# Performance work log

Measured on AMD Instinct MI355X. Metric: run time of the kernel, lower is better.

## Reference

```python
import jax, jax.numpy as jnp
import numpy as np

B, H, C = 131072, 16, 32        # batch, n_holidays, n_changepoints
HID, HP, SKU = 512, 512 // 16, 64  # hidden_dim, hidden per holiday, sku embed dim
TEMP = 0.7
TIME_MAX = 365.0
LN_EPS = 1e-3  # keras LayerNormalization default epsilon


def mish(x):
    return x * jnp.tanh(jax.nn.softplus(x))


def setup_inputs() -> dict:
    key = jax.random.key(0)
    ks = jax.random.split(key, 12)
    inputs = jax.random.uniform(ks[0], (B, H), dtype=jnp.float32) * TIME_MAX
    sku_embedding = jax.random.normal(ks[1], (B, SKU), dtype=jnp.float32)
    # per-holiday params, stacked over holiday axis
    deltas = jnp.full((H, C), TIME_MAX / C, dtype=jnp.float32)  # changepoint_deltas init
    ln_gamma = jnp.ones((H, C), dtype=jnp.float32)
    ln_beta = jnp.zeros((H, C), dtype=jnp.float32)
    attn_w = jax.random.normal(ks[2], (H,), dtype=jnp.float32) * 0.5  # Dense(1) on [...,1]
    Wh = jax.random.normal(ks[3], (H, C, HP), dtype=jnp.float32) * (1.0 / np.sqrt(C))
    Wah = jax.random.normal(ks[4], (HID, HID), dtype=jnp.float32) * (1.0 / np.sqrt(HID))
    Waa = jax.random.normal(ks[5], (HID, HID), dtype=jnp.float32) * (1.0 / np.sqrt(HID))
    Wb = jax.random.normal(ks[6], (SKU, HID), dtype=jnp.float32) * (1.0 / np.sqrt(SKU))
    Wa = jax.random.normal(ks[7], (SKU, HID), dtype=jnp.float32) * (1.0 / np.sqrt(SKU))
    Wo = jax.random.normal(ks[8], (HID, 1), dtype=jnp.float32)
    Wo = Wo / jnp.linalg.norm(Wo, axis=0, keepdims=True)  # UnitNorm(axis=0) constraint
    return {"inputs": inputs, "sku_embedding": sku_embedding, "deltas": deltas,
            "ln_gamma": ln_gamma, "ln_beta": ln_beta, "attn_w": attn_w, "Wh": Wh,
            "Wah": Wah, "Waa": Waa, "Wb": Wb, "Wa": Wa, "Wo": Wo}


def reference(inputs, sku_embedding, deltas, ln_gamma, ln_beta, attn_w, Wh, Wah, Waa, Wb, Wa, Wo):
    # ChangepointReLU (vectorised over holidays): softplus -> cumsum -> rescale to [0, 365]
    pd = jax.nn.softplus(deltas)                     # [H, C]
    cps = jnp.cumsum(pd, axis=-1)
    cps = cps / cps[:, -1:] * TIME_MAX               # time_min = 0
    feats = jax.nn.relu(inputs[:, :, None] - cps[None, :, :])  # [B, H, C]
    # per-holiday LayerNorm over changepoint axis
    mu = jnp.mean(feats, axis=-1, keepdims=True)
    var = jnp.mean((feats - mu) ** 2, axis=-1, keepdims=True)
    normed = (feats - mu) * jax.lax.rsqrt(var + LN_EPS) * ln_gamma[None] + ln_beta[None]
    # per-holiday attention: Dense(1,no bias) on [...,1] == scalar multiply per holiday
    logits = normed * attn_w[None, :, None]
    attn = jax.nn.softmax(logits / TEMP, axis=-1)    # n_changepoints > 1
    attended = normed * attn                          # [B, H, C]
    # per-holiday hidden Dense(HP, mish, no bias), then concat over holidays
    hid = mish(jnp.einsum('bhc,hcd->bhd', attended, Wh))  # [B, H, HP]
    aggregated = hid.reshape(hid.shape[0], H * HP)        # [B, HID]
    agg_hidden = mish(aggregated @ Wah)                   # [B, HID]
    agg_attn = jax.nn.softmax((agg_hidden @ Waa) / TEMP, axis=-1)
    final = agg_hidden * agg_attn                         # dropout inactive (inference)
    beta = jax.nn.sigmoid(sku_embedding @ Wb)
    alpha = sku_embedding @ Wa
    final = final * beta + alpha
    return final @ Wo                                     # [B, 1]
```

## Files before the change

kernel.cpp:

```cpp
#include <hip/hip_runtime.h>
#include <hip/hip_fp16.h>
#include <stdint.h>

#define B_TOT 131072
#define CHUNK 65536
#define NH 16
#define NC 32
#define HIDD 512

typedef unsigned short u16;
typedef unsigned int u32;
typedef __attribute__((ext_vector_type(8))) short short8;
typedef __attribute__((ext_vector_type(4))) float f32x4;
typedef __attribute__((ext_vector_type(4))) int i32x4;

#define GLLDS(g, l) __builtin_amdgcn_global_load_lds((const __attribute__((address_space(1))) unsigned int*)(g), (__attribute__((address_space(3))) unsigned int*)(l), 16, 0, 0)

__device__ __forceinline__ u16 f2bf(float x){
  unsigned u = __float_as_uint(x);
  u += 0x7fffu + ((u >> 16) & 1u);
  return (u16)(u >> 16);
}
__device__ __forceinline__ float bf2f(u16 b){ return __uint_as_float(((unsigned)b) << 16); }
__device__ __forceinline__ u16 f2h(float x){ __half h = __float2half(x); return *(u16*)&h; }
__device__ __forceinline__ float h2f(u16 b){ __half h; *(u16*)&h = b; return __half2float(h); }
__device__ __forceinline__ float mishf(float x){
  float e = __expf(fminf(x, 30.f));
  float u = 1.f + e;
  float u2 = u * u;
  return x * (u2 - 1.f) * __builtin_amdgcn_rcpf(u2 + 1.f);
}

__global__ void prep_small(const float* __restrict__ deltas, const float* __restrict__ Wa,
                           const float* __restrict__ Wo, float* __restrict__ cps, float* __restrict__ wWo)
{
  const int t = threadIdx.x;
  if (t < NH){
    float cum[NC];
    float run = 0.f;
#pragma unroll
    for (int c = 0; c < NC; c++){
      float d = deltas[t*NC + c];
      float sp = (d > 20.f) ? d : log1pf(__expf(d));
      run += sp; cum[c] = run;
    }
    float s = 365.0f / run;
#pragma unroll
    for (int c = 0; c < NC; c++) cps[t*NC + c] = cum[c] * s;
  } else if (t >= 64 && t < 128){
    const int k = t - 64;
    float s = 0.f;
    for (int n = 0; n < HIDD; n++) s += Wa[k*HIDD + n] * Wo[n];
    wWo[k] = s;
  }
}

__global__ void prep_convert(const float* __restrict__ Wah, const float* __restrict__ Waa,
                             const float* __restrict__ Wb, const float* __restrict__ Wh,
                             u16* __restrict__ WahT, u16* __restrict__ WaaT,
                             u16* __restrict__ WbT, u16* __restrict__ WhT)
{
  int i = blockIdx.x * 256 + threadIdx.x;
  if (i < 262144){ int n = i >> 9, k = i & 511; WahT[i] = f2bf(Wah[k*512 + n]); return; }
  i -= 262144;
  if (i < 262144){ int n = i >> 9, k = i & 511; WaaT[i] = f2bf(Waa[k*512 + n]); return; }
  i -= 262144;
  if (i < 32768){ int n = i >> 6, k = i & 63; WbT[i] = f2bf(Wb[k*512 + n]); return; }
  i -= 32768;
  if (i < 16384){ int h = i >> 10, r = i & 1023, d = r >> 5, c = r & 31;
                  WhT[i] = f2bf(Wh[h*1024 + c*32 + d]); return; }
}

__global__ __launch_bounds__(256) void stage1_kernel(
    const float* __restrict__ inputs, const float* __restrict__ sku,
    const float* __restrict__ ln_g, const float* __restrict__ ln_b,
    const float* __restrict__ attnw, const float* __restrict__ cps,
    const float* __restrict__ wWo, const u16* __restrict__ WhT,
    u16* __restrict__ agg, u16* __restrict__ skub, float* __restrict__ skd)
{
  __shared__ __align__(16) float in_l[256];
  __shared__ __align__(16) float cps_l[512];
  __shared__ __align__(16) float gam_l[512];
  __shared__ __align__(16) float bet_l[512];
  __shared__ float aw_l[16];
  __shared__ __align__(16) u16 at_l[16*16*32];
  __shared__ __align__(16) u16 ot_l[16*512];

  const int t = threadIdx.x;
  const int ln = t & 63;
  const long bb = (long)blockIdx.x * 64;

  cps_l[t] = cps[t];       cps_l[t+256] = cps[t+256];
  gam_l[t] = ln_g[t];      gam_l[t+256] = ln_g[t+256];
  bet_l[t] = ln_b[t];      bet_l[t+256] = ln_b[t+256];
  if (t < 16) aw_l[t] = attnw[t];
  in_l[t] = inputs[bb*16 + t];

#pragma unroll
  for (int it = 0; it < 4; it++){
    const long bs = bb + it*16;
    const f32x4 sv = *(const f32x4*)&sku[bs*64 + t*4];
    unsigned lo = (unsigned)f2bf(sv.x) | ((unsigned)f2bf(sv.y) << 16);
    unsigned hi = (unsigned)f2bf(sv.z) | ((unsigned)f2bf(sv.w) << 16);
    unsigned long long v = (unsigned long long)lo | ((unsigned long long)hi << 32);
    *(unsigned long long*)&skub[bs*64 + t*4] = v;
    const f32x4 wv4 = *(const f32x4*)&wWo[(ln & 15)*4];
    float pd = sv.x*wv4.x + sv.y*wv4.y + sv.z*wv4.z + sv.w*wv4.w;
#pragma unroll
    for (int s = 1; s < 16; s <<= 1) pd += __shfl_xor(pd, s);
    if ((ln & 15) == 0) skd[bs + (t >> 4)] = pd;
  }

  const int h = t >> 4, bi = t & 15;
  const int wv = t >> 6;
  const int lrow = ln & 15, lq = ln >> 4;

  short8 wf0[4], wf1[4];
#pragma unroll
  for (int q = 0; q < 4; q++){
    const int hh = wv*4 + q;
    wf0[q] = *(const short8*)&WhT[hh*1024 + lrow*32 + lq*8];
    wf1[q] = *(const short8*)&WhT[hh*1024 + (16 + lrow)*32 + lq*8];
  }
  __syncthreads();

#pragma unroll 1
  for (int it = 0; it < 4; it++){
    const float x = in_l[bi*16 + h];
    const float awv = aw_l[h] * (1.0f/0.7f);
    float nrm[NC];
    float s1 = 0.f;
#pragma unroll
    for (int c = 0; c < NC; c++){ float f = fmaxf(x - cps_l[h*NC + c], 0.f); nrm[c] = f; s1 += f; }
    const float mu = s1 * (1.f/NC);
    float s2 = 0.f;
#pragma unroll
    for (int c = 0; c < NC; c++){ float d = nrm[c] - mu; s2 += d*d; }
    const float rs = rsqrtf(s2 * (1.f/NC) + 1e-3f);
    float lmax = -1e30f;
#pragma unroll
    for (int c = 0; c < NC; c++){
      float nv = (nrm[c] - mu) * rs * gam_l[h*NC + c] + bet_l[h*NC + c];
      nrm[c] = nv;
      lmax = fmaxf(lmax, nv * awv);
    }
    float ps = 0.f;
#pragma unroll
    for (int c = 0; c < NC; c++) ps += __expf(nrm[c]*awv - lmax);
    const float invs = __builtin_amdgcn_rcpf(ps);
#pragma unroll
    for (int c = 0; c < NC; c += 2){
      const float p0 = __expf(nrm[c]*awv - lmax) * invs;
      const float p1 = __expf(nrm[c+1]*awv - lmax) * invs;
      unsigned pk = (unsigned)f2bf(nrm[c]*p0) | ((unsigned)f2bf(nrm[c+1]*p1) << 16);
      *(unsigned*)&at_l[h*512 + bi*32 + c] = pk;
    }
    __syncthreads();

    if (it < 3) in_l[t] = inputs[(bb + (it+1)*16)*16 + t];

#pragma unroll
    for (int q = 0; q < 4; q++){
      const int hh = wv*4 + q;
      short8 af = *(const short8*)&at_l[hh*512 + lrow*32 + lq*8];
      f32x4 acc0 = {0.f,0.f,0.f,0.f}, acc1 = {0.f,0.f,0.f,0.f};
      acc0 = __builtin_amdgcn_mfma_f32_16x16x32_bf16(af, wf0[q], acc0, 0, 0, 0);
      acc1 = __builtin_amdgcn_mfma_f32_16x16x32_bf16(af, wf1[q], acc1, 0, 0, 0);
#pragma unroll
      for (int r = 0; r < 4; r++){
        const int br = lq*4 + r;
        ot_l[br*512 + hh*32 + lrow]      = f2bf(mishf(acc0[r]));
        ot_l[br*512 + hh*32 + 16 + lrow] = f2bf(mishf(acc1[r]));
      }
    }
    __syncthreads();

    {
      const int row = t >> 4, c16 = t & 15;
      const i32x4* src = (const i32x4*)&ot_l[row*512 + c16*32];
      i32x4* dst = (i32x4*)&agg[(bb + it*16 + row)*512 + c16*32];
#pragma unroll
      for (int j = 0; j < 4; j++) dst[j] = src[j];
    }
    __syncthreads();
  }
}

__global__ __launch_bounds__(256, 3) void gemm1(
    const u16* __restrict__ A, const u16* __restrict__ Bt, u16* __restrict__ aggh)
{
  __shared__ __align__(16) u16 smem[24576];
  const int t = threadIdx.x, wv = t >> 6, ln = t & 63;
  const int g = blockIdx.x;
  const int m_idx = (g & 7) + ((g >> 5) << 3);
  const int n_idx = (g >> 3) & 3;
  const long m0 = (long)m_idx * 128;
  const int n0 = n_idx * 128;
  const int lrow = ln & 15, lq = ln >> 4;
  const int wm = wv >> 1, wn = wv & 1;

  auto stage = [&](int buf, int kt){
#pragma unroll
    for (int p = 0; p < 2; p++){
      const int chunk = p*256 + wv*64 + ln;
      const int mm = chunk >> 2, kc = chunk & 3;
      const int kcl = kc ^ ((mm >> 1) & 3);
      GLLDS(&A[(m0 + mm)*512 + kt + kcl*8],  &smem[buf*4096 + (p*256 + wv*64)*8]);
      GLLDS(&Bt[(n0 + mm)*512 + kt + kcl*8], &smem[12288 + buf*4096 + (p*256 + wv*64)*8]);
    }
  };

  f32x4 acc[4][4] = {};
  stage(0, 0); stage(1, 32);
#pragma unroll 1
  for (int ks = 0; ks < 16; ks++){
    const int cur = ks % 3;
    if (ks < 15) asm volatile("s_waitcnt vmcnt(4)" ::: "memory");
    else         asm volatile("s_waitcnt vmcnt(0)" ::: "memory");
    __builtin_amdgcn_s_barrier();
    if (ks + 2 < 16) stage((ks + 2) % 3, (ks + 2)*32);
    short8 a[4], b[4];
#pragma unroll
    for (int i = 0; i < 4; i++){
      const int ra = wm*64 + i*16 + lrow;
      const int rb = wn*64 + i*16 + lrow;
      const int lqa = lq ^ ((ra >> 1) & 3);
      const int lqb = lq ^ ((rb >> 1) & 3);
      a[i] = *(const short8*)&smem[cur*4096 + ra*32 + lqa*8];
      b[i] = *(const short8*)&smem[12288 + cur*4096 + rb*32 + lqb*8];
    }
#pragma unroll
    for (int i = 0; i < 4; i++)
#pragma unroll
      for (int j = 0; j < 4; j++)
        acc[i][j] = __builtin_amdgcn_mfma_f32_16x16x32_bf16(a[i], b[j], acc[i][j], 0, 0, 0);
  }

  const int TP = 136;
  __syncthreads();
#pragma unroll 1
  for (int h = 0; h < 2; h++){
    if (wm == h){
#pragma unroll
      for (int i = 0; i < 4; i++)
#pragma unroll
        for (int j = 0; j < 4; j++)
#pragma unroll
          for (int r = 0; r < 4; r++)
            smem[(i*16 + lq*4 + r)*TP + wn*64 + j*16 + lrow] = f2bf(mishf(acc[i][j][r]));
    }
    __syncthreads();
#pragma unroll
    for (int it = 0; it < 4; it++){
      const int idx = it*256 + t;
      const int row = idx >> 4, ch = idx & 15;
      const i32x4 v = *(const i32x4*)&smem[row*TP + ch*8];
      *(i32x4*)&aggh[(m0 + h*64 + row)*512 + n0 + ch*8] = v;
    }
    __syncthreads();
  }
}

__global__ __launch_bounds__(256, 3) void mega2f(
    const u16* __restrict__ A, const u16* __restrict__ Bt,
    const u16* __restrict__ skub, const u16* __restrict__ WbT,
    const float* __restrict__ Wo, float* __restrict__ part)
{
  __shared__ __align__(16) u16 smem[24576];
  const int t = threadIdx.x, wv = t >> 6, ln = t & 63;
  const int g = blockIdx.x;
  const int m_idx = (g & 7) + ((g >> 5) << 3);
  const int n_idx = (g >> 3) & 3;
  const long m0 = (long)m_idx * 128;
  const int n0 = n_idx * 128;
  const int lrow = ln & 15, lq = ln >> 4;
  const int wm = wv >> 1, wn = wv & 1;
  const float inv_t = 1.0f / 0.7f;

  u32 bwp[4][4][2];
  {
    auto stage3 = [&](int buf, int kt){
#pragma unroll
      for (int p = 0; p < 2; p++){
        const int chunk = p*256 + wv*64 + ln;
        const int mm = chunk >> 2, kc = chunk & 3;
        const int kcl = kc ^ ((mm >> 1) & 3);
        GLLDS(&skub[(m0 + mm)*64 + kt + kcl*8], &smem[buf*4096 + (p*256 + wv*64)*8]);
        GLLDS(&WbT[(n0 + mm)*64 + kt + kcl*8],  &smem[8192 + buf*4096 + (p*256 + wv*64)*8]);
      }
    };
    f32x4 acc3[4][4] = {};
    stage3(0, 0); stage3(1, 32);
    asm volatile("s_waitcnt vmcnt(0)" ::: "memory");
    __builtin_amdgcn_s_barrier();
#pragma unroll
    for (int ks3 = 0; ks3 < 2; ks3++){
      short8 a3[4], b3[4];
#pragma unroll
      for (int i = 0; i < 4; i++){
        const int ra = wm*64 + i*16 + lrow;
        const int rb = wn*64 + i*16 + lrow;
        const int lqa = lq ^ ((ra >> 1) & 3);
        const int lqb = lq ^ ((rb >> 1) & 3);
        a3[i] = *(const short8*)&smem[ks3*4096 + ra*32 + lqa*8];
        b3[i] = *(const short8*)&smem[8192 + ks3*4096 + rb*32 + lqb*8];
      }
#pragma unroll
      for (int i = 0; i < 4; i++)
#pragma unroll
        for (int j = 0; j < 4; j++)
          acc3[i][j] = __builtin_amdgcn_mfma_f32_16x16x32_bf16(a3[i], b3[j], acc3[i][j], 0, 0, 0);
    }
#pragma unroll
    for (int j = 0; j < 4; j++){
      const float wo = Wo[n0 + wn*64 + j*16 + lrow];
#pragma unroll
      for (int i = 0; i < 4; i++)
#pragma unroll
        for (int rp = 0; rp < 2; rp++){
          const float s0 = wo * __builtin_amdgcn_rcpf(1.f + __expf(-acc3[i][j][2*rp]));
          const float s1 = wo * __builtin_amdgcn_rcpf(1.f + __expf(-acc3[i][j][2*rp+1]));
          bwp[i][j][rp] = (u32)f2h(s0) | ((u32)f2h(s1) << 16);
        }
    }
  }
  __syncthreads();

  auto stage = [&](int buf, int kt){
#pragma unroll
    for (int p = 0; p < 2; p++){
      const int chunk = p*256 + wv*64 + ln;
      const int mm = chunk >> 2, kc = chunk & 3;
      const int kcl = kc ^ ((mm >> 1) & 3);
      GLLDS(&A[(m0 + mm)*512 + kt + kcl*8],  &smem[buf*4096 + (p*256 + wv*64)*8]);
      GLLDS(&Bt[(n0 + mm)*512 + kt + kcl*8], &smem[12288 + buf*4096 + (p*256 + wv*64)*8]);
    }
  };

  f32x4 acc[4][4] = {};
  stage(0, 0); stage(1, 32);
#pragma unroll 1
  for (int ks = 0; ks < 16; ks++){
    const int cur = ks % 3;
    if (ks < 15) asm volatile("s_waitcnt vmcnt(4)" ::: "memory");
    else         asm volatile("s_waitcnt vmcnt(0)" ::: "memory");
    __builtin_amdgcn_s_barrier();
    if (ks + 2 < 16) stage((ks + 2) % 3, (ks + 2)*32);
    short8 a[4], b[4];
#pragma unroll
    for (int i = 0; i < 4; i++){
      const int ra = wm*64 + i*16 + lrow;
      const int rb = wn*64 + i*16 + lrow;
      const int lqa = lq ^ ((ra >> 1) & 3);
      const int lqb = lq ^ ((rb >> 1) & 3);
      a[i] = *(const short8*)&smem[cur*4096 + ra*32 + lqa*8];
      b[i] = *(const short8*)&smem[12288 + cur*4096 + rb*32 + lqb*8];
    }
#pragma unroll
    for (int i = 0; i < 4; i++)
#pragma unroll
      for (int j = 0; j < 4; j++)
        acc[i][j] = __builtin_amdgcn_mfma_f32_16x16x32_bf16(a[i], b[j], acc[i][j], 0, 0, 0);
  }

  __syncthreads();
  float* mloc = (float*)smem;
  float* sloc = mloc + 256;
  float* tloc = sloc + 256;

#pragma unroll
  for (int i = 0; i < 4; i++){
#pragma unroll
    for (int r = 0; r < 4; r++){
      float tm = acc[i][0][r];
#pragma unroll
      for (int j = 1; j < 4; j++) tm = fmaxf(tm, acc[i][j][r]);
#pragma unroll
      for (int s = 1; s < 16; s <<= 1) tm = fmaxf(tm, __shfl_xor(tm, s));
      const int rowL = wm*64 + i*16 + lq*4 + r;
      float sp = 0.f, tp = 0.f;
#pragma unroll
      for (int j = 0; j < 4; j++){
        const long gi = (m0 + rowL)*512 + n0 + wn*64 + j*16 + lrow;
        const float e = __expf((acc[i][j][r] - tm) * inv_t);
        const u16 bh = (u16)(bwp[i][j][r >> 1] >> ((r & 1)*16));
        sp += e; tp += e * bf2f(A[gi]) * h2f(bh);
      }
#pragma unroll
      for (int s = 1; s < 16; s <<= 1){ sp += __shfl_xor(sp, s); tp += __shfl_xor(tp, s); }
      if (lrow == 0){
        mloc[rowL*2 + wn] = tm; sloc[rowL*2 + wn] = sp; tloc[rowL*2 + wn] = tp;
      }
    }
  }
  __syncthreads();
  if (t < 128){
    const float ma = mloc[t*2], mb = mloc[t*2 + 1];
    const float M = fmaxf(ma, mb);
    const float wa = __expf((ma - M) * inv_t), wb = __expf((mb - M) * inv_t);
    const float S = sloc[t*2]*wa + sloc[t*2 + 1]*wb;
    const float T = tloc[t*2]*wa + tloc[t*2 + 1]*wb;
    float* pm = part + (size_t)n_idx*3*CHUNK;
    pm[m0 + t]           = M;
    pm[CHUNK + m0 + t]   = S;
    pm[2*CHUNK + m0 + t] = T;
  }
}

__global__ __launch_bounds__(256) void combine_kernel(
    const float* __restrict__ part, const float* __restrict__ skd, float* __restrict__ outp)
{
  const int row = blockIdx.x*256 + threadIdx.x;
  const float inv_t = 1.0f / 0.7f;
  float M = -1e30f;
#pragma unroll
  for (int nt = 0; nt < 4; nt++) M = fmaxf(M, part[(size_t)nt*3*CHUNK + row]);
  float S = 0.f, T = 0.f;
#pragma unroll
  for (int nt = 0; nt < 4; nt++){
    const float w = __expf((part[(size_t)nt*3*CHUNK + row] - M) * inv_t);
    S += part[(size_t)nt*3*CHUNK + CHUNK + row] * w;
    T += part[(size_t)nt*3*CHUNK + 2*CHUNK + row] * w;
  }
  outp[row] = T / S + skd[row];
}

__global__ void ws_too_small(float* o, float v){ o[(long)blockIdx.x*256 + threadIdx.x] = v; }

extern "C" void kernel_launch(void* const* d_in, const int* in_sizes, int n_in,
                              void* d_out, int out_size, void* d_ws, size_t ws_size,
                              hipStream_t stream)
{
  const float* inputs = (const float*)d_in[0];
  const float* sku    = (const float*)d_in[1];
  const float* deltas = (const float*)d_in[2];
  const float* ln_g   = (const float*)d_in[3];
  const float* ln_b   = (const float*)d_in[4];
  const float* attnw  = (const float*)d_in[5];
  const float* Wh     = (const float*)d_in[6];
  const float* Wah    = (const float*)d_in[7];
  const float* Waa    = (const float*)d_in[8];
  const float* Wb     = (const float*)d_in[9];
  const float* Wa     = (const float*)d_in[10];
  const float* Wo     = (const float*)d_in[11];
  float* outp = (float*)d_out;

  const size_t OFF_CPS  = 0;
  const size_t OFF_WWO  = 2048;
  const size_t OFF_WAHT = 4096;
  const size_t OFF_WAAT = OFF_WAHT + 524288;
  const size_t OFF_WBT  = OFF_WAAT + 524288;
  const size_t OFF_WHT  = OFF_WBT  + 65536;
  const size_t OFF_SKUB = OFF_WHT  + 32768;
  const size_t OFF_SKD  = OFF_SKUB + (size_t)CHUNK*64*2;
  const size_t OFF_AGG  = OFF_SKD  + (size_t)CHUNK*4;
  const size_t OFF_AGH  = OFF_AGG  + (size_t)CHUNK*512*2;
  const size_t OFF_PART = OFF_AGH  + (size_t)CHUNK*512*2;
  const size_t NEED     = OFF_PART + (size_t)4*3*CHUNK*4;

  if (ws_size < NEED){
    hipLaunchKernelGGL(ws_too_small, dim3(B_TOT/256), dim3(256), 0, stream,
                       outp, -(float)(ws_size >> 20));
    return;
  }

  char* ws = (char*)d_ws;
  float* cps  = (float*)(ws + OFF_CPS);
  float* wWo  = (float*)(ws + OFF_WWO);
  u16* WahT   = (u16*)(ws + OFF_WAHT);
  u16* WaaT   = (u16*)(ws + OFF_WAAT);
  u16* WbT    = (u16*)(ws + OFF_WBT);
  u16* WhT    = (u16*)(ws + OFF_WHT);
  u16* skub   = (u16*)(ws + OFF_SKUB);
  float* skd  = (float*)(ws + OFF_SKD);
  u16* agg    = (u16*)(ws + OFF_AGG);
  u16* aggh   = (u16*)(ws + OFF_AGH);
  float* part = (float*)(ws + OFF_PART);

  hipLaunchKernelGGL(prep_small, dim3(1), dim3(128), 0, stream, deltas, Wa, Wo, cps, wWo);
  hipLaunchKernelGGL(prep_convert, dim3(2240), dim3(256), 0, stream,
                     Wah, Waa, Wb, Wh, WahT, WaaT, WbT, WhT);

  for (int ch = 0; ch < B_TOT / CHUNK; ch++){
    const float* in_c  = inputs + (size_t)ch * CHUNK * 16;
    const float* sku_c = sku    + (size_t)ch * CHUNK * 64;
    float* out_c       = outp   + (size_t)ch * CHUNK;

    hipLaunchKernelGGL(stage1_kernel, dim3(CHUNK/64), dim3(256), 0, stream,
                       in_c, sku_c, ln_g, ln_b, attnw, cps, wWo, WhT, agg, skub, skd);
    hipLaunchKernelGGL(gemm1, dim3(CHUNK/128*4), dim3(256), 0, stream,
                       agg, WahT, aggh);
    hipLaunchKernelGGL(mega2f, dim3(CHUNK/128*4), dim3(256), 0, stream,
                       aggh, WaaT, skub, WbT, Wo, part);
    hipLaunchKernelGGL(combine_kernel, dim3(CHUNK/256), dim3(256), 0, stream,
                       part, skd, out_c);
  }
}
```

Measured before the change: 452.2 us.

## Enlarge gemm1 to 256x256 tiles with 8 waves and phased pipelining

Rewrites gemm1 to use 256x256 output tiles per 512-thread block instead of 128x128 per 256-thread block. The K loop now takes 64-wide steps, double-buffered, and each step is split into four phases that interleave half-tile global-to-LDS loads with MFMA work, with s_setprio raised around the MFMA bursts. The larger tiles raise arithmetic intensity and cut redundant A/B loads. In exchange the kernel uses 128KB LDS, runs one block per CU, and launches only 512 blocks, which lowers occupancy and could leave some CUs idle.

```diff
diff --git a/kernel.cpp b/kernel.cpp
--- a/kernel.cpp
+++ b/kernel.cpp
@@ -186,80 +186,111 @@
   }
 }
 
-__global__ __launch_bounds__(256, 3) void gemm1(
+#define PHASE(KH, MH) do { \
+  const int buf_ = kt & 1; \
+  const int abase_ = buf_*16384 + (KH)*8192; \
+  const int bbase_ = 32768 + buf_*16384 + (KH)*8192; \
+  short8 a_[4], b_[4]; \
+  _Pragma("unroll") \
+  for (int i = 0; i < 4; i++){ \
+    const int row_ = wm*128 + (MH)*64 + i*16 + lrow; \
+    a_[i] = *(const short8*)&smem[abase_ + row_*32 + (lq ^ ((row_ >> 1) & 3))*8]; \
+    const int nrow_ = wn*64 + i*16 + lrow; \
+    b_[i] = *(const short8*)&smem[bbase_ + nrow_*32 + (lq ^ ((nrow_ >> 1) & 3))*8]; \
+  } \
+  __builtin_amdgcn_s_setprio(1); \
+  _Pragma("unroll") \
+  for (int i = 0; i < 4; i++) \
+    _Pragma("unroll") \
+    for (int j = 0; j < 4; j++) \
+      acc[(MH)*4 + i][j] = __builtin_amdgcn_mfma_f32_16x16x32_bf16(a_[i], b_[j], acc[(MH)*4 + i][j], 0, 0, 0); \
+  __builtin_amdgcn_s_setprio(0); \
+} while(0)
+
+__global__ __launch_bounds__(512, 1) void gemm1(
     const u16* __restrict__ A, const u16* __restrict__ Bt, u16* __restrict__ aggh)
 {
-  __shared__ __align__(16) u16 smem[24576];
-  const int t = threadIdx.x, wv = t >> 6, ln = t & 63;
+  __shared__ __align__(16) u16 smem[65536];
+  const int t = threadIdx.x, wid = t >> 6, ln = t & 63;
+  const int lrow = ln & 15, lq = ln >> 4;
+  const int wm = wid >> 2, wn = wid & 3;
   const int g = blockIdx.x;
-  const int m_idx = (g & 7) + ((g >> 5) << 3);
-  const int n_idx = (g >> 3) & 3;
-  const long m0 = (long)m_idx * 128;
-  const int n0 = n_idx * 128;
-  const int lrow = ln & 15, lq = ln >> 4;
-  const int wm = wv >> 1, wn = wv & 1;
-
-  auto stage = [&](int buf, int kt){
-#pragma unroll
-    for (int p = 0; p < 2; p++){
-      const int chunk = p*256 + wv*64 + ln;
-      const int mm = chunk >> 2, kc = chunk & 3;
-      const int kcl = kc ^ ((mm >> 1) & 3);
-      GLLDS(&A[(m0 + mm)*512 + kt + kcl*8],  &smem[buf*4096 + (p*256 + wv*64)*8]);
-      GLLDS(&Bt[(n0 + mm)*512 + kt + kcl*8], &smem[12288 + buf*4096 + (p*256 + wv*64)*8]);
+  const long m0 = (long)(g >> 1) * 256;
+  const int n0 = (g & 1) * 256;
+
+  auto stageA = [&](int kt_, int kh_){
+#pragma unroll
+    for (int l = 0; l < 2; l++){
+      const int slot = t + l*512;
+      const int row = slot >> 2, kc = slot & 3;
+      const int kcl = kc ^ ((row >> 1) & 3);
+      GLLDS(&A[(m0 + row)*512 + kt_*64 + kh_*32 + kcl*8],
+            &smem[(kt_ & 1)*16384 + kh_*8192 + slot*8]);
     }
   };
-
-  f32x4 acc[4][4] = {};
-  stage(0, 0); stage(1, 32);
+  auto stageB = [&](int kt_, int kh_){
+#pragma unroll
+    for (int l = 0; l < 2; l++){
+      const int slot = t + l*512;
+      const int row = slot >> 2, kc = slot & 3;
+      const int kcl = kc ^ ((row >> 1) & 3);
+      GLLDS(&Bt[(n0 + row)*512 + kt_*64 + kh_*32 + kcl*8],
+            &smem[32768 + (kt_ & 1)*16384 + kh_*8192 + slot*8]);
+    }
+  };
+
+  f32x4 acc[8][4] = {};
+  stageA(0, 0); stageB(0, 0); stageA(0, 1); stageB(0, 1); stageA(1, 0); stageB(1, 0);
+
 #pragma unroll 1
-  for (int ks = 0; ks < 16; ks++){
-    const int cur = ks % 3;
-    if (ks < 15) asm volatile("s_waitcnt vmcnt(4)" ::: "memory");
-    else         asm volatile("s_waitcnt vmcnt(0)" ::: "memory");
+  for (int kt = 0; kt < 8; kt++){
+    if (kt < 7) asm volatile("s_waitcnt vmcnt(8)" ::: "memory");
+    else        asm volatile("s_waitcnt vmcnt(4)" ::: "memory");
     __builtin_amdgcn_s_barrier();
-    if (ks + 2 < 16) stage((ks + 2) % 3, (ks + 2)*32);
-    short8 a[4], b[4];
-#pragma unroll
-    for (int i = 0; i < 4; i++){
-      const int ra = wm*64 + i*16 + lrow;
-      const int rb = wn*64 + i*16 + lrow;
-      const int lqa = lq ^ ((ra >> 1) & 3);
-      const int lqb = lq ^ ((rb >> 1) & 3);
-      a[i] = *(const short8*)&smem[cur*4096 + ra*32 + lqa*8];
-      b[i] = *(const short8*)&smem[12288 + cur*4096 + rb*32 + lqb*8];
-    }
-#pragma unroll
-    for (int i = 0; i < 4; i++)
-#pragma unroll
-      for (int j = 0; j < 4; j++)
-        acc[i][j] = __builtin_amdgcn_mfma_f32_16x16x32_bf16(a[i], b[j], acc[i][j], 0, 0, 0);
-  }
-
-  const int TP = 136;
+    if (kt + 1 < 8) stageA(kt + 1, 1);
+    PHASE(0, 0);
+    __builtin_amdgcn_s_barrier();
+    if (kt + 1 < 8) stageB(kt + 1, 1);
+    PHASE(0, 1);
+    if (kt < 7) asm volatile("s_waitcnt vmcnt(8)" ::: "memory");
+    else        asm volatile("s_waitcnt vmcnt(0)" ::: "memory");
+    __builtin_amdgcn_s_barrier();
+    if (kt + 2 < 8) stageA(kt + 2, 0);
+    PHASE(1, 0);
+    __builtin_amdgcn_s_barrier();
+    if (kt + 2 < 8) stageB(kt + 2, 0);
+    PHASE(1, 1);
+  }
+
   __syncthreads();
+  const int TP = 264;
 #pragma unroll 1
   for (int h = 0; h < 2; h++){
     if (wm == h){
 #pragma unroll
-      for (int i = 0; i < 4; i++)
-#pragma unroll
-        for (int j = 0; j < 4; j++)
-#pragma unroll
-          for (int r = 0; r < 4; r++)
-            smem[(i*16 + lq*4 + r)*TP + wn*64 + j*16 + lrow] = f2bf(mishf(acc[i][j][r]));
+      for (int mh = 0; mh < 2; mh++)
+#pragma unroll
+        for (int i = 0; i < 4; i++)
+#pragma unroll
+          for (int j = 0; j < 4; j++)
+#pragma unroll
+            for (int r = 0; r < 4; r++){
+              const int row = mh*64 + i*16 + lq*4 + r;
+              smem[row*TP + wn*64 + j*16 + lrow] = f2bf(mishf(acc[mh*4 + i][j][r]));
+            }
     }
     __syncthreads();
 #pragma unroll
-    for (int it = 0; it < 4; it++){
-      const int idx = it*256 + t;
-      const int row = idx >> 4, ch = idx & 15;
+    for (int it = 0; it < 8; it++){
+      const int idx = it*512 + t;
+      const int row = idx >> 5, ch = idx & 31;
       const i32x4 v = *(const i32x4*)&smem[row*TP + ch*8];
-      *(i32x4*)&aggh[(m0 + h*64 + row)*512 + n0 + ch*8] = v;
+      *(i32x4*)&aggh[(m0 + h*128 + row)*512 + n0 + ch*8] = v;
     }
     __syncthreads();
   }
 }
+#undef PHASE
 
 __global__ __launch_bounds__(256, 3) void mega2f(
     const u16* __restrict__ A, const u16* __restrict__ Bt,
@@ -488,7 +519,7 @@
 
     hipLaunchKernelGGL(stage1_kernel, dim3(CHUNK/64), dim3(256), 0, stream,
                        in_c, sku_c, ln_g, ln_b, attnw, cps, wWo, WhT, agg, skub, skd);
-    hipLaunchKernelGGL(gemm1, dim3(CHUNK/128*4), dim3(256), 0, stream,
+    hipLaunchKernelGGL(gemm1, dim3(CHUNK/256*2), dim3(512), 0, stream,
                        agg, WahT, aggh);
     hipLaunchKernelGGL(mega2f, dim3(CHUNK/128*4), dim3(256), 0, stream,
                        aggh, WaaT, skub, WbT, Wo, part);
```

New measurement: 465.9 us. 1.03x slower.
